# Performance work log

Measured on AMD Instinct MI355X. Metric: run time of the kernel, lower is better.

The kernel has to match this reference:

```python
import jax, jax.numpy as jnp
import numpy as np

B, T, C, H = 32, 512, 256, 8
DEG = 16
EPS = 1e-5


def setup_inputs() -> dict:
    rs = np.random.RandomState(0)
    counts = rs.randint(384, 513, size=B)  # ragged graph sizes, max 512 = T
    N = int(counts.sum())
    E = N * DEG
    # dense-batch scatter indices: node i of graph b -> slot b*T + rank
    idx = np.concatenate([b * T + np.arange(c) for b, c in enumerate(counts)]).astype(np.int64)
    mask = np.zeros((B, T), dtype=bool)
    for b, c in enumerate(counts):
        mask[b, :c] = True
    key = jax.random.key(0)
    ks = jax.random.split(key, 12)
    w = lambda k, shape: jax.random.normal(k, shape, jnp.float32) * 0.02
    z = lambda n: jnp.zeros((n,), jnp.float32)
    o = lambda n: jnp.ones((n,), jnp.float32)
    return dict(
        x=jax.random.normal(ks[0], (N, C), jnp.float32),
        edge_index=jax.random.randint(ks[1], (2, E), 0, N),
        idx=jnp.asarray(idx), mask=jnp.asarray(mask),
        W_root=w(ks[2], (C, C)), W_nbr=w(ks[3], (C, C)), b_conv=z(C),
        Wq=w(ks[4], (C, C)), Wk=w(ks[5], (C, C)), Wv=w(ks[6], (C, C)),
        bq=z(C), bk=z(C), bv=z(C), Wo=w(ks[7], (C, C)), bo=z(C),
        W1=w(ks[8], (C, 2 * C)), b1=z(2 * C), W2=w(ks[9], (2 * C, C)), b2=z(C),
        g1=o(C), be1=z(C), g2=o(C), be2=z(C), g3=o(C), be3=z(C),
    )


def _bn(h, g, b):
    # BatchNorm1d over nodes (training-mode batch stats, biased variance)
    m = h.mean(0)
    v = h.var(0)
    return g * (h - m) * jax.lax.rsqrt(v + EPS) + b


def _forward(x, W_root, W_nbr, b_conv, Wq, Wk, Wv, bq, bk, bv, Wo, bo,
             W1, b1, W2, b2, g1, be1, g2, be2, g3, be3,
             edge_index, idx, mask):
    N = x.shape[0]
    # --- local MPNN (GraphConv): x_i W_root + (sum_{j->i} x_j) W_nbr + b ---
    agg = jax.ops.segment_sum(x[edge_index[0]], edge_index[1], num_segments=N)
    h_local = x @ W_root + agg @ W_nbr + b_conv
    h_local = _bn(h_local + x, g1, be1)  # dropout p=0, residual, norm1
    # --- to_dense_batch: scatter ragged nodes into [B, T, C] ---
    xd = jnp.zeros((B * T, C), x.dtype).at[idx].set(x).reshape(B, T, C)
    # --- global MHA with key_padding_mask = ~mask ---
    Dh = C // H
    q = (xd @ Wq + bq).reshape(B, T, H, Dh)
    k = (xd @ Wk + bk).reshape(B, T, H, Dh)
    v = (xd @ Wv + bv).reshape(B, T, H, Dh)
    scores = jnp.einsum('bqhd,bkhd->bhqk', q, k) * (1.0 / float(np.sqrt(Dh)))
    scores = jnp.where(mask[:, None, None, :], scores, -1e9)
    attn = jax.nn.softmax(scores, axis=-1)
    o = jnp.einsum('bhqk,bkhd->bqhd', attn, v).reshape(B, T, C)
    o = o @ Wo + bo
    # --- unpad (index_select on flattened mask) + residual + norm2 ---
    h_attn = o.reshape(B * T, C)[idx] + x
    h_attn = _bn(h_attn, g2, be2)
    # --- combine branches, MLP with residual, norm3 ---
    out = h_local + h_attn
    out = out + jax.nn.relu(out @ W1 + b1) @ W2 + b2
    return _bn(out, g3, be3)


def reference(x, edge_index, idx, mask, W_root, W_nbr, b_conv, Wq, Wk, Wv,
              bq, bk, bv, Wo, bo, W1, b1, W2, b2,
              g1, be1, g2, be2, g3, be3):
    return _forward(x, W_root, W_nbr, b_conv, Wq, Wk, Wv, bq, bk, bv, Wo, bo,
                    W1, b1, W2, b2, g1, be1, g2, be2, g3, be3,
                    edge_index, idx, mask)
```

## Files before the change

### kernel.cpp

```cpp
#include <hip/hip_runtime.h>
#include <hip/hip_bf16.h>
#include <math.h>

#define Bc 32
#define Tc 512
#define Cc 256
#define Hc 8
#define BT (Bc * Tc)
#define EPS 1e-5f
#define LDAP 40
#define CSTRIDE 128

typedef __bf16 bf16x8 __attribute__((ext_vector_type(8)));
typedef float f32x4 __attribute__((ext_vector_type(4)));
typedef unsigned short us8_t __attribute__((ext_vector_type(8)));

__device__ inline unsigned short f2bf(float f) {
    unsigned int u = __float_as_uint(f);
    u += 0x7fffu + ((u >> 16) & 1u);
    return (unsigned short)(u >> 16);
}
__device__ inline unsigned short f2bf_fast(float f) {
    __bf16 h = (__bf16)f;
    return __builtin_bit_cast(unsigned short, h);
}
__device__ inline float bf2f(unsigned short u) {
    return __uint_as_float((unsigned int)u << 16);
}

__global__ void wcvt_fused_kernel(const float* __restrict__ Wr, const float* __restrict__ Wn,
                                  const float* __restrict__ Wq, const float* __restrict__ Wk,
                                  const float* __restrict__ Wv, const float* __restrict__ Wo,
                                  const float* __restrict__ W1, const float* __restrict__ W2,
                                  const float* __restrict__ bq, const float* __restrict__ bk,
                                  const float* __restrict__ bv,
                                  unsigned short* __restrict__ wsq, float* __restrict__ bqkv,
                                  const float* __restrict__ x, const int* __restrict__ idx,
                                  unsigned short* __restrict__ x_bf,
                                  unsigned short* __restrict__ xd_bf,
                                  int* __restrict__ bcnt, int* __restrict__ zbase,
                                  int N, int nzero4) {
    const float scale = 0.17677669529663687f;
    int gid = blockIdx.x * 256 + threadIdx.x;
    const int X0 = 656128 + N * 32;
    const int XZ = X0 + 64;
    if (gid >= XZ) {
        int j = gid - XZ;
        if (j < nzero4) {
            int4 z = {0, 0, 0, 0};
            *(int4*)&zbase[j * 4] = z;
        }
        return;
    }
    if (gid >= X0) {
        int b = gid - X0;
        if (b >= 32) return;
        int lo = 0, hi = N, v0 = b << 9;
        while (lo < hi) { int mid = (lo + hi) >> 1; if (idx[mid] < v0) lo = mid + 1; else hi = mid; }
        int s = lo;
        lo = 0; hi = N; int v1 = (b + 1) << 9;
        while (lo < hi) { int mid = (lo + hi) >> 1; if (idx[mid] < v1) lo = mid + 1; else hi = mid; }
        bcnt[b] = lo - s;
        return;
    }
    if (gid >= 656128) {
        int j = gid - 656128;
        int i = j >> 5;
        if (i >= N) return;
        int c8 = (j & 31) * 8;
        const float* sp = x + (size_t)i * Cc + c8;
        float4 f0 = *(const float4*)sp;
        float4 f1 = *(const float4*)(sp + 4);
        us8_t pk;
        pk[0] = f2bf_fast(f0.x); pk[1] = f2bf_fast(f0.y);
        pk[2] = f2bf_fast(f0.z); pk[3] = f2bf_fast(f0.w);
        pk[4] = f2bf_fast(f1.x); pk[5] = f2bf_fast(f1.y);
        pk[6] = f2bf_fast(f1.z); pk[7] = f2bf_fast(f1.w);
        *(us8_t*)&x_bf[(size_t)i * Cc + c8] = pk;
        int slot = idx[i];
        *(us8_t*)&xd_bf[(size_t)slot * Cc + c8] = pk;
        return;
    }
    if (gid >= 655360) {
        int j = gid - 655360;
        bqkv[j] = (j < 256) ? bq[j] * scale : (j < 512 ? bk[j - 256] : bv[j - 512]);
        return;
    }
    const float* src; int base, K, N_; float mul = 1.f;
    if (gid < 65536)       { src = Wr; base = 0;      K = 256; N_ = 256; }
    else if (gid < 131072) { src = Wn; base = 65536;  K = 256; N_ = 256; }
    else if (gid < 196608) { src = Wq; base = 131072; K = 256; N_ = 256; mul = scale; }
    else if (gid < 262144) { src = Wk; base = 196608; K = 256; N_ = 256; }
    else if (gid < 327680) { src = Wv; base = 262144; K = 256; N_ = 256; }
    else if (gid < 393216) { src = Wo; base = 327680; K = 256; N_ = 256; }
    else if (gid < 524288) { src = W1; base = 393216; K = 256; N_ = 512; }
    else                   { src = W2; base = 524288; K = 512; N_ = 256; }
    int loc = gid - base;
    int n = loc / K, k = loc % K;
    wsq[gid] = f2bf(src[(size_t)k * N_ + n] * mul);
}

__global__ void fill_csr_kernel(const int* __restrict__ ei, int* __restrict__ cursor,
                                int* __restrict__ csr, int E) {
    int e = blockIdx.x * 256 + threadIdx.x;
    if (e >= E) return;
    int dst = ei[E + e];
    int pos = atomicAdd(&cursor[dst], 1);
    if (pos < CSTRIDE) csr[(size_t)dst * CSTRIDE + pos] = ei[e];
}

__global__ __launch_bounds__(256) void gather_kernel(const unsigned short* __restrict__ x_bf,
                                                     const int* __restrict__ csr,
                                                     const int* __restrict__ cursor,
                                                     unsigned short* __restrict__ agg_bf,
                                                     int N) {
    int i = blockIdx.x * 4 + (threadIdx.x >> 6);
    if (i >= N) return;
    int l4 = (threadIdx.x & 63) * 4;
    int dcount = cursor[i];
    if (dcount > CSTRIDE) dcount = CSTRIDE;
    const int* row = csr + (size_t)i * CSTRIDE;
    f32x4 a0 = {0.f, 0.f, 0.f, 0.f}, a1 = a0, a2 = a0, a3 = a0;
    int e = 0;
    for (; e + 4 <= dcount; e += 4) {
        int i0 = row[e + 0];
        int i1 = row[e + 1];
        int i2 = row[e + 2];
        int i3 = row[e + 3];
        ushort4 u0 = *(const ushort4*)(x_bf + (size_t)i0 * Cc + l4);
        ushort4 u1 = *(const ushort4*)(x_bf + (size_t)i1 * Cc + l4);
        ushort4 u2 = *(const ushort4*)(x_bf + (size_t)i2 * Cc + l4);
        ushort4 u3 = *(const ushort4*)(x_bf + (size_t)i3 * Cc + l4);
        a0[0] += bf2f(u0.x); a0[1] += bf2f(u0.y); a0[2] += bf2f(u0.z); a0[3] += bf2f(u0.w);
        a1[0] += bf2f(u1.x); a1[1] += bf2f(u1.y); a1[2] += bf2f(u1.z); a1[3] += bf2f(u1.w);
        a2[0] += bf2f(u2.x); a2[1] += bf2f(u2.y); a2[2] += bf2f(u2.z); a2[3] += bf2f(u2.w);
        a3[0] += bf2f(u3.x); a3[1] += bf2f(u3.y); a3[2] += bf2f(u3.z); a3[3] += bf2f(u3.w);
    }
    for (; e < dcount; ++e) {
        ushort4 u = *(const ushort4*)(x_bf + (size_t)row[e] * Cc + l4);
        a0[0] += bf2f(u.x); a0[1] += bf2f(u.y); a0[2] += bf2f(u.z); a0[3] += bf2f(u.w);
    }
    f32x4 s = (a0 + a1) + (a2 + a3);
    ushort4 w4;
    w4.x = f2bf_fast(s[0]); w4.y = f2bf_fast(s[1]);
    w4.z = f2bf_fast(s[2]); w4.w = f2bf_fast(s[3]);
    *(ushort4*)&agg_bf[(size_t)i * Cc + l4] = w4;
}

template <bool RELU, bool OUTBF16, bool STATS>
__device__ __forceinline__ void gemm_body(
    const unsigned short* __restrict__ A, const int* __restrict__ gidx,
    const unsigned short* __restrict__ Bt,
    const unsigned short* __restrict__ A2, const unsigned short* __restrict__ B2t,
    const float* __restrict__ bias, const float* __restrict__ res,
    void* __restrict__ Cout, float* __restrict__ stats, int M, int K, int Nc,
    int bx, int by, unsigned short* As, unsigned short* Bs) {
    int tid = threadIdx.x;
    int row0 = by * 128;
    int col0 = bx * 64;
    int lane = tid & 63;
    int w = tid >> 6;
    int wr = (w >> 1) * 64;
    int wc = (w & 1) * 32;
    int fr = lane & 15;
    int kk = (lane >> 4) * 8;

    f32x4 acc[4][2] = {};

    int npass = (A2 != nullptr) ? 2 : 1;
    for (int pass = 0; pass < npass; ++pass) {
        const unsigned short* Ap = pass ? A2 : A;
        const unsigned short* Bp = pass ? B2t : Bt;
        int r = tid >> 1;
        int kc = (tid & 1) * 16;
        int ar = row0 + r;
        if (ar >= M) ar = M - 1;
        int arr = gidx ? gidx[ar] : ar;
        const unsigned short* abase = Ap + (size_t)arr * K + kc;
        int bc = tid >> 2;
        int bkc = (tid & 3) * 8;
        const unsigned short* bbase = Bp + (size_t)(col0 + bc) * K + bkc;
        for (int k0 = 0; k0 < K; k0 += 32) {
            __syncthreads();
            *(us8_t*)&As[r * LDAP + kc] = *(const us8_t*)(abase + k0);
            *(us8_t*)&As[r * LDAP + kc + 8] = *(const us8_t*)(abase + k0 + 8);
            *(us8_t*)&Bs[bc * LDAP + bkc] = *(const us8_t*)(bbase + k0);
            __syncthreads();
            bf16x8 bf0 = *(bf16x8*)&Bs[(wc + fr) * LDAP + kk];
            bf16x8 bf1 = *(bf16x8*)&Bs[(wc + 16 + fr) * LDAP + kk];
#pragma unroll
            for (int fm = 0; fm < 4; ++fm) {
                bf16x8 af = *(bf16x8*)&As[(wr + fm * 16 + fr) * LDAP + kk];
                acc[fm][0] = __builtin_amdgcn_mfma_f32_16x16x32_bf16(af, bf0, acc[fm][0], 0, 0, 0);
                acc[fm][1] = __builtin_amdgcn_mfma_f32_16x16x32_bf16(af, bf1, acc[fm][1], 0, 0, 0);
            }
        }
    }
    int rq = (lane >> 4) * 4;
    float cs[2] = {0.f, 0.f}, cq[2] = {0.f, 0.f};
#pragma unroll
    for (int fm = 0; fm < 4; ++fm) {
#pragma unroll
        for (int fn = 0; fn < 2; ++fn) {
            int col = col0 + wc + fn * 16 + fr;
#pragma unroll
            for (int i = 0; i < 4; ++i) {
                int row = row0 + wr + fm * 16 + rq + i;
                if (row < M) {
                    float v = acc[fm][fn][i];
                    if (bias) v += bias[col];
                    if (res) v += res[(size_t)row * Nc + col];
                    if (RELU) v = fmaxf(v, 0.f);
                    if (OUTBF16)
                        ((unsigned short*)Cout)[(size_t)row * Nc + col] = f2bf_fast(v);
                    else
                        ((float*)Cout)[(size_t)row * Nc + col] = v;
                    if (STATS) { cs[fn] += v; cq[fn] += v * v; }
                }
            }
        }
    }
    if (STATS) {
#pragma unroll
        for (int fn = 0; fn < 2; ++fn) {
            cs[fn] += __shfl_xor(cs[fn], 16); cs[fn] += __shfl_xor(cs[fn], 32);
            cq[fn] += __shfl_xor(cq[fn], 16); cq[fn] += __shfl_xor(cq[fn], 32);
        }
        if ((lane >> 4) == 0) {
            int col = col0 + wc + fr;
            atomicAdd(&stats[col], cs[0]);
            atomicAdd(&stats[256 + col], cq[0]);
            atomicAdd(&stats[col + 16], cs[1]);
            atomicAdd(&stats[256 + col + 16], cq[1]);
        }
    }
}

template <bool RELU, bool OUTBF16, bool STATS>
__global__ __launch_bounds__(256) void gemm_mfma_kernel(
    const unsigned short* A, const int* gidx, const unsigned short* Bt,
    const unsigned short* A2, const unsigned short* B2t,
    const float* bias, const float* res, void* Cout, float* stats,
    int M, int K, int Nc) {
    __shared__ unsigned short As[128 * LDAP];
    __shared__ unsigned short Bs[64 * LDAP];
    gemm_body<RELU, OUTBF16, STATS>(A, gidx, Bt, A2, B2t, bias, res, Cout, stats,
                                    M, K, Nc, blockIdx.x, blockIdx.y, As, Bs);
}

__global__ __launch_bounds__(256) void convqkv_kernel(
    const unsigned short* __restrict__ x_bf, const unsigned short* __restrict__ agg_bf,
    const unsigned short* __restrict__ Wrt, const unsigned short* __restrict__ Wnt,
    const unsigned short* __restrict__ Wqkvt,
    const float* __restrict__ b_conv, const float* __restrict__ x,
    float* __restrict__ hB, float* __restrict__ stats,
    const unsigned short* __restrict__ xd_bf, const float* __restrict__ bqkv,
    unsigned short* __restrict__ qkvb, int N, int convBlocks) {
    __shared__ unsigned short As[128 * LDAP];
    __shared__ unsigned short Bs[64 * LDAP];
    int blk = blockIdx.x;
    if (blk < convBlocks) {
        gemm_body<false, false, true>(x_bf, nullptr, Wrt, agg_bf, Wnt, b_conv, x,
                                      hB, stats, N, 256, 256, blk & 3, blk >> 2, As, Bs);
    } else {
        int q = blk - convBlocks;
        gemm_body<false, true, false>(xd_bf, nullptr, Wqkvt, nullptr, nullptr, bqkv, nullptr,
                                      qkvb, nullptr, BT, 256, 768, q % 12, q / 12, As, Bs);
    }
}

__global__ void bn_apply_kernel(const float* __restrict__ in, float* __restrict__ out,
                                const float* __restrict__ g, const float* __restrict__ be,
                                const float* __restrict__ stats, int M) {
    int gid = blockIdx.x * 256 + threadIdx.x;
    if (gid >= M * Cc) return;
    int c = gid & (Cc - 1);
    float invM = 1.f / (float)M;
    float mean = stats[c] * invM;
    float var = stats[Cc + c] * invM - mean * mean;
    float sc = g[c] * rsqrtf(var + EPS);
    out[gid] = (in[gid] - mean) * sc + be[c];
}

__global__ void bn12_apply_kernel(const float* __restrict__ hpre,
                                  const float* __restrict__ hattn,
                                  const float* __restrict__ g1, const float* __restrict__ be1,
                                  const float* __restrict__ g2, const float* __restrict__ be2,
                                  const float* __restrict__ stats,
                                  float* __restrict__ out, unsigned short* __restrict__ out_bf,
                                  int M) {
    int gid = blockIdx.x * 256 + threadIdx.x;
    if (gid >= M * Cc) return;
    int c = gid & (Cc - 1);
    float invM = 1.f / (float)M;
    float mean1 = stats[c] * invM;
    float var1 = stats[Cc + c] * invM - mean1 * mean1;
    float sc1 = g1[c] * rsqrtf(var1 + EPS);
    float mean2 = stats[2 * Cc + c] * invM;
    float var2 = stats[3 * Cc + c] * invM - mean2 * mean2;
    float sc2 = g2[c] * rsqrtf(var2 + EPS);
    float v = (hpre[gid] - mean1) * sc1 + be1[c] + (hattn[gid] - mean2) * sc2 + be2[c];
    out[gid] = v;
    out_bf[gid] = f2bf_fast(v);
}

__global__ __launch_bounds__(256) void attn_mfma_kernel(const unsigned short* __restrict__ qkvb,
                                                        const int* __restrict__ bcnt,
                                                        unsigned short* __restrict__ o_bf) {
    const int blk = ((blockIdx.x & 7) << 7) | ((int)blockIdx.x >> 3);
    const int qt = blk & 3;
    const int bh = blk >> 2;
    const int b = bh >> 3;
    const int h = bh & 7;
    const int tid = threadIdx.x;
    const int lane = tid & 63;
    const int w = tid >> 6;
    const int fr = lane & 15;
    const int g = lane >> 4;
    const int kk = g * 8;
    const int q0 = qt * 128 + w * 32;

    __shared__ unsigned short Ks[32 * LDAP];
    __shared__ unsigned short Vt[32 * LDAP];
    __shared__ unsigned short Pl[4][2][16 * LDAP];

    const int count = bcnt[b];

    const unsigned short* qp = qkvb + (size_t)(b * Tc + q0 + fr) * 768 + h * 32 + kk;
    bf16x8 qa0 = *(const bf16x8*)qp;
    bf16x8 qa1 = *(const bf16x8*)(qp + (size_t)16 * 768);

    f32x4 op00 = {0.f, 0.f, 0.f, 0.f}, op01 = op00;
    f32x4 op10 = op00, op11 = op00;
    float l0 = 0.f, l1 = 0.f;
    float m0 = -1e30f, m1 = -1e30f;

    const int nt = (count + 31) >> 5;
    for (int t = 0; t < nt; ++t) {
        const int kbase = t * 32;
        __syncthreads();
        {
            int key = tid >> 3;
            int d4 = (tid & 7) * 4;
            const unsigned short* kp =
                qkvb + (size_t)(b * Tc + kbase + key) * 768 + 256 + h * 32 + d4;
            *(ushort4*)&Ks[key * LDAP + d4] = *(const ushort4*)kp;
        }
        {
            int vkey = tid & 31;
            int d0 = (tid >> 5) * 4;
            const unsigned short* vp =
                qkvb + (size_t)(b * Tc + kbase + vkey) * 768 + 512 + h * 32 + d0;
            ushort4 vv = *(const ushort4*)vp;
            Vt[(d0 + 0) * LDAP + vkey] = vv.x;
            Vt[(d0 + 1) * LDAP + vkey] = vv.y;
            Vt[(d0 + 2) * LDAP + vkey] = vv.z;
            Vt[(d0 + 3) * LDAP + vkey] = vv.w;
        }
        __syncthreads();

        bf16x8 ka0 = *(bf16x8*)&Ks[fr * LDAP + kk];
        bf16x8 ka1 = *(bf16x8*)&Ks[(16 + fr) * LDAP + kk];
        f32x4 z = {0.f, 0.f, 0.f, 0.f};
        f32x4 s00 = __builtin_amdgcn_mfma_f32_16x16x32_bf16(ka0, qa0, z, 0, 0, 0);
        f32x4 s10 = __builtin_amdgcn_mfma_f32_16x16x32_bf16(ka1, qa0, z, 0, 0, 0);
        f32x4 s01 = __builtin_amdgcn_mfma_f32_16x16x32_bf16(ka0, qa1, z, 0, 0, 0);
        f32x4 s11 = __builtin_amdgcn_mfma_f32_16x16x32_bf16(ka1, qa1, z, 0, 0, 0);

#pragma unroll
        for (int i = 0; i < 4; ++i) {
            bool v0 = (kbase + g * 4 + i) < count;
            bool v1 = (kbase + 16 + g * 4 + i) < count;
            s00[i] = v0 ? s00[i] : -1e30f;
            s01[i] = v0 ? s01[i] : -1e30f;
            s10[i] = v1 ? s10[i] : -1e30f;
            s11[i] = v1 ? s11[i] : -1e30f;
        }

        float r0_ = fmaxf(fmaxf(fmaxf(s00[0], s00[1]), fmaxf(s00[2], s00[3])),
                          fmaxf(fmaxf(s10[0], s10[1]), fmaxf(s10[2], s10[3])));
        r0_ = fmaxf(r0_, __shfl_xor(r0_, 16));
        r0_ = fmaxf(r0_, __shfl_xor(r0_, 32));
        float mn0 = fmaxf(m0, r0_);
        float c0 = __expf(m0 - mn0);
        m0 = mn0;
        l0 *= c0;
        float p00[4], p10[4];
#pragma unroll
        for (int i = 0; i < 4; ++i) {
            p00[i] = __expf(s00[i] - mn0);
            p10[i] = __expf(s10[i] - mn0);
            l0 += p00[i] + p10[i];
        }
        float r1_ = fmaxf(fmaxf(fmaxf(s01[0], s01[1]), fmaxf(s01[2], s01[3])),
                          fmaxf(fmaxf(s11[0], s11[1]), fmaxf(s11[2], s11[3])));
        r1_ = fmaxf(r1_, __shfl_xor(r1_, 16));
        r1_ = fmaxf(r1_, __shfl_xor(r1_, 32));
        float mn1 = fmaxf(m1, r1_);
        float c1 = __expf(m1 - mn1);
        m1 = mn1;
        l1 *= c1;
        float p01[4], p11[4];
#pragma unroll
        for (int i = 0; i < 4; ++i) {
            p01[i] = __expf(s01[i] - mn1);
            p11[i] = __expf(s11[i] - mn1);
            l1 += p01[i] + p11[i];
        }

        unsigned short* pw0 = &Pl[w][0][0];
        unsigned short* pw1 = &Pl[w][1][0];
        ushort4 q00, q10, q01, q11;
        q00.x = f2bf_fast(p00[0]); q00.y = f2bf_fast(p00[1]);
        q00.z = f2bf_fast(p00[2]); q00.w = f2bf_fast(p00[3]);
        q10.x = f2bf_fast(p10[0]); q10.y = f2bf_fast(p10[1]);
        q10.z = f2bf_fast(p10[2]); q10.w = f2bf_fast(p10[3]);
        q01.x = f2bf_fast(p01[0]); q01.y = f2bf_fast(p01[1]);
        q01.z = f2bf_fast(p01[2]); q01.w = f2bf_fast(p01[3]);
        q11.x = f2bf_fast(p11[0]); q11.y = f2bf_fast(p11[1]);
        q11.z = f2bf_fast(p11[2]); q11.w = f2bf_fast(p11[3]);
        *(ushort4*)&pw0[fr * LDAP + g * 4] = q00;
        *(ushort4*)&pw0[fr * LDAP + 16 + g * 4] = q10;
        *(ushort4*)&pw1[fr * LDAP + g * 4] = q01;
        *(ushort4*)&pw1[fr * LDAP + 16 + g * 4] = q11;

#pragma unroll
        for (int i = 0; i < 4; ++i) {
            float ci0 = __shfl(c0, g * 4 + i);
            float ci1 = __shfl(c1, g * 4 + i);
            op00[i] *= ci0; op01[i] *= ci0;
            op10[i] *= ci1; op11[i] *= ci1;
        }

        asm volatile("s_waitcnt lgkmcnt(0)" ::: "memory");
        __builtin_amdgcn_sched_barrier(0);

        bf16x8 pa0 = *(bf16x8*)&pw0[fr * LDAP + kk];
        bf16x8 pa1 = *(bf16x8*)&pw1[fr * LDAP + kk];
        bf16x8 vb0 = *(bf16x8*)&Vt[fr * LDAP + kk];
        bf16x8 vb1 = *(bf16x8*)&Vt[(16 + fr) * LDAP + kk];
        op00 = __builtin_amdgcn_mfma_f32_16x16x32_bf16(pa0, vb0, op00, 0, 0, 0);
        op01 = __builtin_amdgcn_mfma_f32_16x16x32_bf16(pa0, vb1, op01, 0, 0, 0);
        op10 = __builtin_amdgcn_mfma_f32_16x16x32_bf16(pa1, vb0, op10, 0, 0, 0);
        op11 = __builtin_amdgcn_mfma_f32_16x16x32_bf16(pa1, vb1, op11, 0, 0, 0);
    }

    l0 += __shfl_xor(l0, 16); l0 += __shfl_xor(l0, 32);
    l1 += __shfl_xor(l1, 16); l1 += __shfl_xor(l1, 32);
    float inv0 = 1.f / l0;
    float inv1 = 1.f / l1;
#pragma unroll
    for (int i = 0; i < 4; ++i) {
        float li0 = __shfl(inv0, g * 4 + i);
        float li1 = __shfl(inv1, g * 4 + i);
        size_t row0 = (size_t)(b * Tc + q0 + g * 4 + i);
        size_t row1 = row0 + 16;
        o_bf[row0 * Cc + h * 32 + fr] = f2bf_fast(op00[i] * li0);
        o_bf[row0 * Cc + h * 32 + 16 + fr] = f2bf_fast(op01[i] * li0);
        o_bf[row1 * Cc + h * 32 + fr] = f2bf_fast(op10[i] * li1);
        o_bf[row1 * Cc + h * 32 + 16 + fr] = f2bf_fast(op11[i] * li1);
    }
}

extern "C" void kernel_launch(void* const* d_in, const int* in_sizes, int n_in,
                              void* d_out, int out_size, void* d_ws, size_t ws_size,
                              hipStream_t stream) {
    const float* x      = (const float*)d_in[0];
    const int*   ei     = (const int*)d_in[1];
    const int*   idx    = (const int*)d_in[2];
    const float* W_root = (const float*)d_in[4];
    const float* W_nbr  = (const float*)d_in[5];
    const float* b_conv = (const float*)d_in[6];
    const float* Wq     = (const float*)d_in[7];
    const float* Wk     = (const float*)d_in[8];
    const float* Wv     = (const float*)d_in[9];
    const float* bq     = (const float*)d_in[10];
    const float* bk     = (const float*)d_in[11];
    const float* bv     = (const float*)d_in[12];
    const float* Wo     = (const float*)d_in[13];
    const float* bo     = (const float*)d_in[14];
    const float* W1     = (const float*)d_in[15];
    const float* b1     = (const float*)d_in[16];
    const float* W2     = (const float*)d_in[17];
    const float* b2     = (const float*)d_in[18];
    const float* g1     = (const float*)d_in[19];
    const float* be1    = (const float*)d_in[20];
    const float* g2     = (const float*)d_in[21];
    const float* be2    = (const float*)d_in[22];
    const float* g3     = (const float*)d_in[23];
    const float* be3    = (const float*)d_in[24];

    const int N = in_sizes[0] / Cc;
    const int E = in_sizes[1] / 2;

    float* ws = (float*)d_ws;
    float* hB    = ws;
    float* bqkv  = hB + (size_t)N * Cc;
    unsigned short* wsq    = (unsigned short*)(bqkv + 768);
    unsigned short* x_bf   = wsq + 655360;
    unsigned short* hB_bf  = x_bf + (size_t)N * Cc;
    unsigned short* hid_bf = hB_bf + (size_t)N * Cc;
    unsigned short* xd_bf  = hid_bf + (size_t)N * 2 * Cc;
    unsigned short* qkvb   = xd_bf + (size_t)BT * Cc;
    int*   bcnt   = (int*)(qkvb + (size_t)BT * 768);
    float* stats  = (float*)(bcnt + 32);
    int*   cursor = (int*)(stats + 6 * Cc);
    int*   csr    = cursor + N;
    float* bufA   = (float*)d_out;
    unsigned short* agg_bf = (unsigned short*)d_out;
    unsigned short* ao = xd_bf;

    const unsigned short* Wrt   = wsq;
    const unsigned short* Wnt   = wsq + 65536;
    const unsigned short* Wqkvt = wsq + 131072;
    const unsigned short* Wot   = wsq + 327680;
    const unsigned short* W1t   = wsq + 393216;
    const unsigned short* W2t   = wsq + 524288;

    const int nzero = 6 * Cc + N;
    const int nzero4 = (nzero + 3) / 4;

    {
        int total = 656128 + N * 32 + 64 + nzero4;
        wcvt_fused_kernel<<<(total + 255) / 256, 256, 0, stream>>>(
            W_root, W_nbr, Wq, Wk, Wv, Wo, W1, W2, bq, bk, bv, wsq, bqkv,
            x, idx, x_bf, xd_bf, bcnt, (int*)stats, N, nzero4);
    }

    fill_csr_kernel<<<(E + 255) / 256, 256, 0, stream>>>(ei, cursor, csr, E);

    gather_kernel<<<(N + 3) / 4, 256, 0, stream>>>(x_bf, csr, cursor, agg_bf, N);

    {
        int convBlocks = 4 * ((N + 127) / 128);
        int qkvBlocks = 12 * (BT / 128);
        convqkv_kernel<<<convBlocks + qkvBlocks, 256, 0, stream>>>(
            x_bf, agg_bf, Wrt, Wnt, Wqkvt, b_conv, x, hB, stats,
            xd_bf, bqkv, qkvb, N, convBlocks);
    }

    attn_mfma_kernel<<<Bc * Hc * 4, 256, 0, stream>>>(qkvb, bcnt, ao);

    {
        dim3 grid(Cc / 64, (N + 127) / 128);
        gemm_mfma_kernel<false, false, true><<<grid, 256, 0, stream>>>(
            ao, idx, Wot, nullptr, nullptr, bo, x, bufA, stats + 2 * Cc, N, Cc, Cc);
    }

    bn12_apply_kernel<<<(N * Cc + 255) / 256, 256, 0, stream>>>(
        hB, bufA, g1, be1, g2, be2, stats, hB, hB_bf, N);

    {
        dim3 grid(512 / 64, (N + 127) / 128);
        gemm_mfma_kernel<true, true, false><<<grid, 256, 0, stream>>>(
            hB_bf, nullptr, W1t, nullptr, nullptr, b1, nullptr, hid_bf, nullptr, N, Cc, 512);
    }

    {
        dim3 grid(Cc / 64, (N + 127) / 128);
        gemm_mfma_kernel<false, false, true><<<grid, 256, 0, stream>>>(
            hid_bf, nullptr, W2t, nullptr, nullptr, b2, hB, bufA, stats + 4 * Cc, N, 512, Cc);
    }

    bn_apply_kernel<<<(N * Cc + 255) / 256, 256, 0, stream>>>(
        bufA, bufA, g3, be3, stats + 4 * Cc, N);
}
```

Measured before the change: 226.4 us.

## Widen GEMM tiles to 128x128 with swizzled LDS and register prefetch

Doubles the GEMM tile width from 64 to 128 columns, so each wave computes a 64x64 sub-tile with 16 MFMA accumulators and reuses each A fragment across four B fragments. The padded LDS layout is replaced with an XOR-swizzled 32-element row stride to avoid bank conflicts. The next K-slice of global data is prefetched into registers while MFMAs run on the current one. All launch grids are halved to match. Costs are higher register pressure and fewer blocks, which could lower occupancy and leave some CUs idle on the smaller GEMMs.

```diff
diff --git a/kernel.cpp b/kernel.cpp
--- a/kernel.cpp
+++ b/kernel.cpp
@@ -9,6 +9,7 @@
 #define BT (Bc * Tc)
 #define EPS 1e-5f
 #define LDAP 40
+#define LDSW 32
 #define CSTRIDE 128
 
 typedef __bf16 bf16x8 __attribute__((ext_vector_type(8)));
@@ -157,51 +158,72 @@
     int bx, int by, unsigned short* As, unsigned short* Bs) {
     int tid = threadIdx.x;
     int row0 = by * 128;
-    int col0 = bx * 64;
+    int col0 = bx * 128;
     int lane = tid & 63;
     int w = tid >> 6;
     int wr = (w >> 1) * 64;
-    int wc = (w & 1) * 32;
+    int wc = (w & 1) * 64;
     int fr = lane & 15;
-    int kk = (lane >> 4) * 8;
-
-    f32x4 acc[4][2] = {};
+    int g = lane >> 4;
+
+    f32x4 acc[4][4] = {};
+
+    int r = tid >> 1;
+    int c0 = (tid & 1) * 2;
+    int kc = c0 * 8;
+    int so0 = r * LDSW + ((c0 ^ (r & 3)) << 3);
+    int so1 = r * LDSW + (((c0 + 1) ^ (r & 3)) << 3);
 
     int npass = (A2 != nullptr) ? 2 : 1;
     for (int pass = 0; pass < npass; ++pass) {
         const unsigned short* Ap = pass ? A2 : A;
         const unsigned short* Bp = pass ? B2t : Bt;
-        int r = tid >> 1;
-        int kc = (tid & 1) * 16;
         int ar = row0 + r;
         if (ar >= M) ar = M - 1;
         int arr = gidx ? gidx[ar] : ar;
         const unsigned short* abase = Ap + (size_t)arr * K + kc;
-        int bc = tid >> 2;
-        int bkc = (tid & 3) * 8;
-        const unsigned short* bbase = Bp + (size_t)(col0 + bc) * K + bkc;
+        const unsigned short* bbase = Bp + (size_t)(col0 + r) * K + kc;
+        us8_t pa0 = *(const us8_t*)(abase);
+        us8_t pa1 = *(const us8_t*)(abase + 8);
+        us8_t pb0 = *(const us8_t*)(bbase);
+        us8_t pb1 = *(const us8_t*)(bbase + 8);
         for (int k0 = 0; k0 < K; k0 += 32) {
             __syncthreads();
-            *(us8_t*)&As[r * LDAP + kc] = *(const us8_t*)(abase + k0);
-            *(us8_t*)&As[r * LDAP + kc + 8] = *(const us8_t*)(abase + k0 + 8);
-            *(us8_t*)&Bs[bc * LDAP + bkc] = *(const us8_t*)(bbase + k0);
+            *(us8_t*)&As[so0] = pa0;
+            *(us8_t*)&As[so1] = pa1;
+            *(us8_t*)&Bs[so0] = pb0;
+            *(us8_t*)&Bs[so1] = pb1;
             __syncthreads();
-            bf16x8 bf0 = *(bf16x8*)&Bs[(wc + fr) * LDAP + kk];
-            bf16x8 bf1 = *(bf16x8*)&Bs[(wc + 16 + fr) * LDAP + kk];
+            int k1 = k0 + 32;
+            if (k1 < K) {
+                pa0 = *(const us8_t*)(abase + k1);
+                pa1 = *(const us8_t*)(abase + k1 + 8);
+                pb0 = *(const us8_t*)(bbase + k1);
+                pb1 = *(const us8_t*)(bbase + k1 + 8);
+            }
+            bf16x8 bfr[4];
+#pragma unroll
+            for (int fn = 0; fn < 4; ++fn) {
+                int br = wc + fn * 16 + fr;
+                bfr[fn] = *(bf16x8*)&Bs[br * LDSW + ((g ^ (br & 3)) << 3)];
+            }
 #pragma unroll
             for (int fm = 0; fm < 4; ++fm) {
-                bf16x8 af = *(bf16x8*)&As[(wr + fm * 16 + fr) * LDAP + kk];
-                acc[fm][0] = __builtin_amdgcn_mfma_f32_16x16x32_bf16(af, bf0, acc[fm][0], 0, 0, 0);
-                acc[fm][1] = __builtin_amdgcn_mfma_f32_16x16x32_bf16(af, bf1, acc[fm][1], 0, 0, 0);
+                int arow = wr + fm * 16 + fr;
+                bf16x8 af = *(bf16x8*)&As[arow * LDSW + ((g ^ (arow & 3)) << 3)];
+#pragma unroll
+                for (int fn = 0; fn < 4; ++fn)
+                    acc[fm][fn] =
+                        __builtin_amdgcn_mfma_f32_16x16x32_bf16(af, bfr[fn], acc[fm][fn], 0, 0, 0);
             }
         }
     }
-    int rq = (lane >> 4) * 4;
-    float cs[2] = {0.f, 0.f}, cq[2] = {0.f, 0.f};
+    int rq = g * 4;
+    float cs[4] = {0.f, 0.f, 0.f, 0.f}, cq[4] = {0.f, 0.f, 0.f, 0.f};
 #pragma unroll
     for (int fm = 0; fm < 4; ++fm) {
 #pragma unroll
-        for (int fn = 0; fn < 2; ++fn) {
+        for (int fn = 0; fn < 4; ++fn) {
             int col = col0 + wc + fn * 16 + fr;
 #pragma unroll
             for (int i = 0; i < 4; ++i) {
@@ -222,16 +244,17 @@
     }
     if (STATS) {
 #pragma unroll
-        for (int fn = 0; fn < 2; ++fn) {
+        for (int fn = 0; fn < 4; ++fn) {
             cs[fn] += __shfl_xor(cs[fn], 16); cs[fn] += __shfl_xor(cs[fn], 32);
             cq[fn] += __shfl_xor(cq[fn], 16); cq[fn] += __shfl_xor(cq[fn], 32);
         }
-        if ((lane >> 4) == 0) {
-            int col = col0 + wc + fr;
-            atomicAdd(&stats[col], cs[0]);
-            atomicAdd(&stats[256 + col], cq[0]);
-            atomicAdd(&stats[col + 16], cs[1]);
-            atomicAdd(&stats[256 + col + 16], cq[1]);
+        if (g == 0) {
+#pragma unroll
+            for (int fn = 0; fn < 4; ++fn) {
+                int col = col0 + wc + fn * 16 + fr;
+                atomicAdd(&stats[col], cs[fn]);
+                atomicAdd(&stats[256 + col], cq[fn]);
+            }
         }
     }
 }
@@ -242,8 +265,8 @@
     const unsigned short* A2, const unsigned short* B2t,
     const float* bias, const float* res, void* Cout, float* stats,
     int M, int K, int Nc) {
-    __shared__ unsigned short As[128 * LDAP];
-    __shared__ unsigned short Bs[64 * LDAP];
+    __shared__ unsigned short As[128 * LDSW];
+    __shared__ unsigned short Bs[128 * LDSW];
     gemm_body<RELU, OUTBF16, STATS>(A, gidx, Bt, A2, B2t, bias, res, Cout, stats,
                                     M, K, Nc, blockIdx.x, blockIdx.y, As, Bs);
 }
@@ -256,16 +279,16 @@
     float* __restrict__ hB, float* __restrict__ stats,
     const unsigned short* __restrict__ xd_bf, const float* __restrict__ bqkv,
     unsigned short* __restrict__ qkvb, int N, int convBlocks) {
-    __shared__ unsigned short As[128 * LDAP];
-    __shared__ unsigned short Bs[64 * LDAP];
+    __shared__ unsigned short As[128 * LDSW];
+    __shared__ unsigned short Bs[128 * LDSW];
     int blk = blockIdx.x;
     if (blk < convBlocks) {
         gemm_body<false, false, true>(x_bf, nullptr, Wrt, agg_bf, Wnt, b_conv, x,
-                                      hB, stats, N, 256, 256, blk & 3, blk >> 2, As, Bs);
+                                      hB, stats, N, 256, 256, blk & 1, blk >> 1, As, Bs);
     } else {
         int q = blk - convBlocks;
         gemm_body<false, true, false>(xd_bf, nullptr, Wqkvt, nullptr, nullptr, bqkv, nullptr,
-                                      qkvb, nullptr, BT, 256, 768, q % 12, q / 12, As, Bs);
+                                      qkvb, nullptr, BT, 256, 768, q % 6, q / 6, As, Bs);
     }
 }
 
@@ -532,8 +555,8 @@
     gather_kernel<<<(N + 3) / 4, 256, 0, stream>>>(x_bf, csr, cursor, agg_bf, N);
 
     {
-        int convBlocks = 4 * ((N + 127) / 128);
-        int qkvBlocks = 12 * (BT / 128);
+        int convBlocks = 2 * ((N + 127) / 128);
+        int qkvBlocks = 6 * (BT / 128);
         convqkv_kernel<<<convBlocks + qkvBlocks, 256, 0, stream>>>(
             x_bf, agg_bf, Wrt, Wnt, Wqkvt, b_conv, x, hB, stats,
             xd_bf, bqkv, qkvb, N, convBlocks);
@@ -542,7 +565,7 @@
     attn_mfma_kernel<<<Bc * Hc * 4, 256, 0, stream>>>(qkvb, bcnt, ao);
 
     {
-        dim3 grid(Cc / 64, (N + 127) / 128);
+        dim3 grid(Cc / 128, (N + 127) / 128);
         gemm_mfma_kernel<false, false, true><<<grid, 256, 0, stream>>>(
             ao, idx, Wot, nullptr, nullptr, bo, x, bufA, stats + 2 * Cc, N, Cc, Cc);
     }
@@ -551,13 +574,13 @@
         hB, bufA, g1, be1, g2, be2, stats, hB, hB_bf, N);
 
     {
-        dim3 grid(512 / 64, (N + 127) / 128);
+        dim3 grid(512 / 128, (N + 127) / 128);
         gemm_mfma_kernel<true, true, false><<<grid, 256, 0, stream>>>(
             hB_bf, nullptr, W1t, nullptr, nullptr, b1, nullptr, hid_bf, nullptr, N, Cc, 512);
     }
 
     {
-        dim3 grid(Cc / 64, (N + 127) / 128);
+        dim3 grid(Cc / 128, (N + 127) / 128);
         gemm_mfma_kernel<false, false, true><<<grid, 256, 0, stream>>>(
             hid_bf, nullptr, W2t, nullptr, nullptr, b2, hB, bufA, stats + 4 * Cc, N, 512, Cc);
     }
```

Measured after the change: 259.0 us. 1.14x slower.
